# Kernel tuning notes

Measured on AMD Instinct MI355X. Metric: run time of the kernel, lower is better.

The kernel has to match this reference:

```python
import jax, jax.numpy as jnp
import numpy as np

N_NODES = 50000
IN_C = 128
OUT_C = 128
EDGE_F = 65
N_EDGES = 800000
EDGE_ATTR_COLS = 70


def setup_inputs() -> dict:
    key = jax.random.key(0)
    ks = jax.random.split(key, 10)
    fcat = 3 * IN_C + EDGE_F
    sc = lambda d: 1.0 / np.sqrt(d)
    return {
        "x": jax.random.normal(ks[0], (N_NODES, IN_C), dtype=jnp.float32),
        "edge_index": jax.random.randint(ks[1], (2, N_EDGES), 0, N_NODES, dtype=jnp.int32),
        "edge_attr": jax.random.normal(ks[2], (N_EDGES, EDGE_ATTR_COLS), dtype=jnp.float32),
        # f_linear: Linear(fcat -> IN_C, bias=True) followed by ELU
        "Wf": jax.random.normal(ks[3], (fcat, IN_C), dtype=jnp.float32) * sc(fcat),
        "bf": jnp.zeros((IN_C,), dtype=jnp.float32),
        # q/k linears: Linear(IN_C -> IN_C, bias=False)
        "Wq": jax.random.normal(ks[4], (IN_C, IN_C), dtype=jnp.float32) * sc(IN_C),
        "Wk": jax.random.normal(ks[5], (IN_C, IN_C), dtype=jnp.float32) * sc(IN_C),
        # alinear: Linear(IN_C -> 1, bias=False) + Tanh
        "Wa": jax.random.normal(ks[6], (IN_C, 1), dtype=jnp.float32) * sc(IN_C),
        # updatalinear: Linear(IN_C -> OUT_C, bias=True)
        "Wu": jax.random.normal(ks[7], (IN_C, OUT_C), dtype=jnp.float32) * sc(IN_C),
        "bu": jnp.zeros((OUT_C,), dtype=jnp.float32),
    }


def reference(x, edge_index, edge_attr, Wf, bf, Wq, Wk, Wa, Wu, bu):
    src = edge_index[0]
    tgt = edge_index[1]
    # message: gather endpoints, concat with delta and edge features, fuse MLP
    ni = x[src]                      # [E, C]
    nj = x[tgt]                      # [E, C]
    mask = (edge_attr[:, 0:1] < 8).astype(x.dtype)  # [E, 1]
    fcat = jnp.concatenate([ni, nj, ni - nj, edge_attr[:, :EDGE_F]], axis=1)
    f = jax.nn.elu(fcat @ Wf + bf) * mask           # [E, C]
    scale = IN_C ** (-0.5)
    q = ni @ Wq                                      # [E, C]
    k = f @ Wk                                       # [E, C]
    a = jnp.tanh((q * k * scale) @ Wa)               # [E, 1]
    # NOTE: faithful to source: denominator = exp(sum(a)), not sum(exp(a))
    numerator = jnp.exp(a)
    a_sum = jax.ops.segment_sum(a, src, num_segments=N_NODES)   # [N, 1]
    denominator = jnp.exp(a_sum)[src]                            # [E, 1]
    s = numerator / denominator
    z = s * f                                        # [E, C]
    # aggregate: scatter-sum over source nodes
    aggr = jax.ops.segment_sum(z, src, num_segments=N_NODES)     # [N, C]
    # update
    return (x + aggr) @ Wu + bu
```

## Files before the change

### kernel.cpp

```cpp
#include <hip/hip_runtime.h>

#define E_EDGES 800000
#define NN 50000
#define C 128
#define EAC 70
#define EF 65
#define SCALE 0.08838834764831845f

typedef __attribute__((ext_vector_type(8))) short short8;
typedef __attribute__((ext_vector_type(4))) float floatx4;

__device__ __forceinline__ unsigned short f2bf(float f) {
  unsigned u = __builtin_bit_cast(unsigned, f);
  unsigned r = (u + 0x7FFFu + ((u >> 16) & 1u)) >> 16;
  return (unsigned short)r;
}
__device__ __forceinline__ float bf2f(unsigned short h) {
  unsigned u = ((unsigned)h) << 16;
  return __builtin_bit_cast(float, u);
}

__global__ void setup_kernel(const float* __restrict__ Wf, const float* __restrict__ Wq,
                             const float* __restrict__ Wk, const float* __restrict__ Wa,
                             const int* __restrict__ src, unsigned short* __restrict__ wfrag,
                             float* __restrict__ Wm, int* __restrict__ deg) {
  int b = blockIdx.x;
  if (b < 64) {
    int idx = b * 256 + threadIdx.x;
    int r = idx >> 7, d = idx & 127;
    const float* wq = Wq + (size_t)r * C;
    const float* wk = Wk + (size_t)d * C;
    float s = 0.f;
    for (int c = 0; c < C; ++c) s += wq[c] * Wa[c] * wk[c];
    Wm[idx] = s * SCALE;
  } else if (b < 240) {
    int idx = (b - 64) * 256 + threadIdx.x;
    int arr = idx >> 14;
    int rem = idx & 16383;
    int j = rem & 7;
    int l = (rem >> 3) & 63;
    int st = rem >> 9;
    int s = st >> 3, t = st & 7;
    int k = s * 32 + (l >> 4) * 8 + j;
    int n = t * 16 + (l & 15);
    float v;
    if (arr == 0)      v = Wf[k * C + n] + Wf[(256 + k) * C + n];
    else if (arr == 1) v = Wf[(128 + k) * C + n] - Wf[(256 + k) * C + n];
    else               v = (k < EF) ? Wf[(384 + k) * C + n] : 0.f;
    wfrag[idx] = f2bf(v);
  } else {
    int e = (b - 240) * 256 + threadIdx.x;
    atomicAdd(deg + src[e], 1);
  }
}

__global__ __launch_bounds__(256) void m_kernel(const float* __restrict__ x,
                                                const float* __restrict__ Wm,
                                                unsigned short* __restrict__ M,
                                                unsigned short* __restrict__ XB) {
  __shared__ float rows[32][129];
  int b0 = blockIdx.x * 32;
  for (int idx = threadIdx.x; idx < 32 * 128; idx += 256) {
    int r = idx >> 7, i = idx & 127;
    int n = b0 + r;
    float v = 0.f;
    if (n < NN) {
      v = x[(size_t)n * C + i];
      XB[(size_t)n * C + i] = f2bf(v);
    }
    rows[r][i] = v;
  }
  __syncthreads();
  int tr = threadIdx.x >> 4;
  int tc = threadIdx.x & 15;
  floatx4 a00 = (floatx4){0,0,0,0}, a01 = a00, a10 = a00, a11 = a00;
  for (int i = 0; i < C; ++i) {
    float r0 = rows[tr * 2][i], r1 = rows[tr * 2 + 1][i];
    const floatx4* wr = (const floatx4*)(Wm + (size_t)i * C + tc * 8);
    floatx4 w0 = wr[0], w1 = wr[1];
    a00 += w0 * r0; a01 += w1 * r0;
    a10 += w0 * r1; a11 += w1 * r1;
  }
  int n0 = b0 + tr * 2;
  for (int rr = 0; rr < 2; ++rr) {
    int n = n0 + rr;
    if (n < NN) {
      floatx4 v0 = rr ? a10 : a00, v1 = rr ? a11 : a01;
      short8 o;
      for (int j = 0; j < 4; ++j) { o[j] = (short)f2bf(v0[j]); o[4 + j] = (short)f2bf(v1[j]); }
      *(short8*)(M + (size_t)n * C + tc * 8) = o;
    }
  }
}

__global__ __launch_bounds__(1024) void scan_kernel(const int* __restrict__ deg,
                                                    int* __restrict__ offs) {
  __shared__ int buf[1024];
  const int CH = 49;
  int t = threadIdx.x, base = t * CH;
  int s = 0;
  for (int k = 0; k < CH; ++k)
    if (base + k < NN) s += deg[base + k];
  buf[t] = s;
  __syncthreads();
  for (int d = 1; d < 1024; d <<= 1) {
    int add = (t >= d) ? buf[t - d] : 0;
    __syncthreads();
    buf[t] += add;
    __syncthreads();
  }
  int excl = buf[t] - s;
  for (int k = 0; k < CH; ++k)
    if (base + k < NN) { offs[base + k] = excl; excl += deg[base + k]; }
}

__global__ void pos_kernel(const int* __restrict__ src, const int* __restrict__ tgt,
                           const int* __restrict__ offs, int* __restrict__ cursor,
                           int* __restrict__ perm, int* __restrict__ srcs,
                           int* __restrict__ tgts) {
  int e = blockIdx.x * 256 + threadIdx.x;
  int r = src[e];
  int p = offs[r] + atomicAdd(cursor + r, 1);
  perm[p] = e;
  srcs[p] = r;
  tgts[p] = tgt[e];
}

__global__ __launch_bounds__(256, 5) void edge_kernel(
    const unsigned short* __restrict__ XB, const float* __restrict__ ea,
    const float* __restrict__ bfv, const unsigned short* __restrict__ wfrag,
    const int* __restrict__ perm, const int* __restrict__ srcs,
    const int* __restrict__ tgts, const unsigned short* __restrict__ M,
    unsigned short* __restrict__ Z, float* __restrict__ A) {
  __shared__ unsigned short f_lds[4][16][136];
  __shared__ float mask_lds[4][16];
  const int l = threadIdx.x & 63;
  const int w = threadIdx.x >> 6;
  const int lo = l & 15, quad = l >> 4;
  const int e0 = (blockIdx.x * 4 + w) * 16;

  const short8* WF1 = (const short8*)wfrag;
  const short8* WF2 = (const short8*)(wfrag + 16384);
  const short8* WF4 = (const short8*)(wfrag + 32768);

  int p = e0 + lo;
  int sp = srcs[p], tp = tgts[p], ep = perm[p];

  short8 niF[4], njF[4], eaF[3];
  {
    const short8* xr = (const short8*)(XB + (size_t)sp * C);
    const short8* yr = (const short8*)(XB + (size_t)tp * C);
    for (int s = 0; s < 4; ++s) { niF[s] = xr[s * 4 + quad]; njF[s] = yr[s * 4 + quad]; }
  }
  {
    const float* er = ea + (size_t)ep * EAC;
    const float2* ca = (const float2*)(er + quad * 8);
    const float2* cb = (const float2*)(er + 32 + quad * 8);
    float2 a0 = ca[0], a1 = ca[1], a2 = ca[2], a3 = ca[3];
    float2 b0 = cb[0], b1 = cb[1], b2 = cb[2], b3 = cb[3];
    short8 t0, t1, t2;
    t0[0] = (short)f2bf(a0.x); t0[1] = (short)f2bf(a0.y);
    t0[2] = (short)f2bf(a1.x); t0[3] = (short)f2bf(a1.y);
    t0[4] = (short)f2bf(a2.x); t0[5] = (short)f2bf(a2.y);
    t0[6] = (short)f2bf(a3.x); t0[7] = (short)f2bf(a3.y);
    t1[0] = (short)f2bf(b0.x); t1[1] = (short)f2bf(b0.y);
    t1[2] = (short)f2bf(b1.x); t1[3] = (short)f2bf(b1.y);
    t1[4] = (short)f2bf(b2.x); t1[5] = (short)f2bf(b2.y);
    t1[6] = (short)f2bf(b3.x); t1[7] = (short)f2bf(b3.y);
    for (int j = 0; j < 8; ++j) t2[j] = 0;
    if (quad == 0) {
      t2[0] = (short)f2bf(er[64]);
      mask_lds[w][lo] = (a0.x < 8.f) ? 1.f : 0.f;
    }
    eaF[0] = t0; eaF[1] = t1; eaF[2] = t2;
  }

  float maskv[4];
  int srcRow[4];
  for (int i = 0; i < 4; ++i) {
    maskv[i] = mask_lds[w][quad * 4 + i];
    srcRow[i] = srcs[e0 + quad * 4 + i];
  }

  for (int t = 0; t < 8; ++t) {
    floatx4 acc = (floatx4){0.f, 0.f, 0.f, 0.f};
    for (int s = 0; s < 4; ++s)
      acc = __builtin_amdgcn_mfma_f32_16x16x32_bf16(niF[s], WF1[(s * 8 + t) * 64 + l], acc, 0, 0, 0);
    for (int s = 0; s < 4; ++s)
      acc = __builtin_amdgcn_mfma_f32_16x16x32_bf16(njF[s], WF2[(s * 8 + t) * 64 + l], acc, 0, 0, 0);
    for (int s = 0; s < 3; ++s)
      acc = __builtin_amdgcn_mfma_f32_16x16x32_bf16(eaF[s], WF4[(s * 8 + t) * 64 + l], acc, 0, 0, 0);
    float bias = bfv[lo + 16 * t];
    for (int i = 0; i < 4; ++i) {
      float v = acc[i] + bias;
      v = v > 0.f ? v : expm1f(v);
      v *= maskv[i];
      f_lds[w][quad * 4 + i][lo + 16 * t] = f2bf(v);
    }
  }

  for (int i = 0; i < 4; ++i) {
    int pc = e0 + quad * 4 + i;
    const short8 fv = *(const short8*)&f_lds[w][quad * 4 + i][lo * 8];
    const short8 mv = *(const short8*)(M + (size_t)srcRow[i] * C + lo * 8);
    float d = 0.f;
    for (int j = 0; j < 8; ++j)
      d += bf2f((unsigned short)fv[j]) * bf2f((unsigned short)mv[j]);
    d += __shfl_xor(d, 1);
    d += __shfl_xor(d, 2);
    d += __shfl_xor(d, 4);
    d += __shfl_xor(d, 8);
    float a = tanhf(d);
    float cf = expf(a);
    short8 zv;
    for (int j = 0; j < 8; ++j) zv[j] = (short)f2bf(cf * bf2f((unsigned short)fv[j]));
    *(short8*)(Z + (size_t)pc * C + lo * 8) = zv;
    if (lo == 0) A[pc] = a;
  }
}

__global__ __launch_bounds__(256) void gather_node_kernel(
    const float* __restrict__ x, const unsigned short* __restrict__ Z,
    const float* __restrict__ A, const int* __restrict__ offs,
    const int* __restrict__ deg, const float* __restrict__ Wu,
    const float* __restrict__ bu, float* __restrict__ out) {
  __shared__ float rows[32][129];
  int b0 = blockIdx.x * 32;
  int w = threadIdx.x >> 6, l = threadIdx.x & 63;
  for (int r = w; r < 32; r += 4) {
    int n = b0 + r;
    if (n < NN) {
      int beg = offs[n], dn = deg[n];
      float ax = 0.f, ay = 0.f, asum = 0.f;
      const unsigned short* zp = Z + (size_t)beg * C + l * 2;
      const float* ap = A + beg;
      int j = 0;
      for (; j + 1 < dn; j += 2) {
        ushort2 z0 = *(const ushort2*)zp;
        ushort2 z1 = *(const ushort2*)(zp + C);
        zp += 2 * C;
        asum += ap[j] + ap[j + 1];
        ax += bf2f(z0.x) + bf2f(z1.x);
        ay += bf2f(z0.y) + bf2f(z1.y);
      }
      if (j < dn) {
        ushort2 z0 = *(const ushort2*)zp;
        asum += ap[j];
        ax += bf2f(z0.x); ay += bf2f(z0.y);
      }
      float cf = expf(-asum);
      rows[r][l * 2]     = x[(size_t)n * C + l * 2]     + cf * ax;
      rows[r][l * 2 + 1] = x[(size_t)n * C + l * 2 + 1] + cf * ay;
    } else {
      rows[r][l * 2] = 0.f;
      rows[r][l * 2 + 1] = 0.f;
    }
  }
  __syncthreads();
  int tr = threadIdx.x >> 4;
  int tc = threadIdx.x & 15;
  floatx4 a00 = (floatx4){0,0,0,0}, a01 = a00, a10 = a00, a11 = a00;
  for (int i = 0; i < C; ++i) {
    float r0 = rows[tr * 2][i], r1 = rows[tr * 2 + 1][i];
    const floatx4* wr = (const floatx4*)(Wu + (size_t)i * C + tc * 8);
    floatx4 w0 = wr[0], w1 = wr[1];
    a00 += w0 * r0; a01 += w1 * r0;
    a10 += w0 * r1; a11 += w1 * r1;
  }
  const floatx4* bv = (const floatx4*)(bu + tc * 8);
  floatx4 bb0 = bv[0], bb1 = bv[1];
  int n0 = b0 + tr * 2;
  if (n0 < NN) {
    floatx4* o = (floatx4*)(out + (size_t)n0 * C + tc * 8);
    o[0] = a00 + bb0; o[1] = a01 + bb1;
  }
  if (n0 + 1 < NN) {
    floatx4* o = (floatx4*)(out + (size_t)(n0 + 1) * C + tc * 8);
    o[0] = a10 + bb0; o[1] = a11 + bb1;
  }
}

__global__ __launch_bounds__(256, 4) void fb_edge_kernel(
    const float* __restrict__ x, const int* __restrict__ src,
    const int* __restrict__ tgt, const float* __restrict__ ea,
    const float* __restrict__ bfv, const unsigned short* __restrict__ wfrag,
    const unsigned short* __restrict__ M, float* __restrict__ a_sum,
    float* __restrict__ P) {
  __shared__ unsigned short f_lds[4][16][136];
  __shared__ float mask_lds[4][16];
  const int l = threadIdx.x & 63;
  const int w = threadIdx.x >> 6;
  const int lo = l & 15, quad = l >> 4;
  const int e0 = (blockIdx.x * 4 + w) * 16;
  const short8* WF1 = (const short8*)wfrag;
  const short8* WF2 = (const short8*)(wfrag + 16384);
  const short8* WF4 = (const short8*)(wfrag + 32768);

  int p = e0 + lo;
  int sp = src[p], tp = tgt[p];
  short8 niF[4], njF[4], eaF[3];
  {
    const float* xr = x + (size_t)sp * C;
    const float* yr = x + (size_t)tp * C;
    for (int s = 0; s < 4; ++s) {
      int kb = s * 32 + quad * 8;
      const floatx4* xv = (const floatx4*)(xr + kb);
      const floatx4* yv = (const floatx4*)(yr + kb);
      floatx4 x0 = xv[0], x1 = xv[1], y0 = yv[0], y1 = yv[1];
      short8 a, b;
      for (int j = 0; j < 4; ++j) { a[j] = (short)f2bf(x0[j]); a[4 + j] = (short)f2bf(x1[j]); }
      for (int j = 0; j < 4; ++j) { b[j] = (short)f2bf(y0[j]); b[4 + j] = (short)f2bf(y1[j]); }
      niF[s] = a; njF[s] = b;
    }
    const float* er = ea + (size_t)p * EAC;
    const float2* ca = (const float2*)(er + quad * 8);
    const float2* cb = (const float2*)(er + 32 + quad * 8);
    float2 a0 = ca[0], a1 = ca[1], a2 = ca[2], a3 = ca[3];
    float2 b0 = cb[0], b1 = cb[1], b2 = cb[2], b3 = cb[3];
    short8 t0, t1, t2;
    t0[0] = (short)f2bf(a0.x); t0[1] = (short)f2bf(a0.y);
    t0[2] = (short)f2bf(a1.x); t0[3] = (short)f2bf(a1.y);
    t0[4] = (short)f2bf(a2.x); t0[5] = (short)f2bf(a2.y);
    t0[6] = (short)f2bf(a3.x); t0[7] = (short)f2bf(a3.y);
    t1[0] = (short)f2bf(b0.x); t1[1] = (short)f2bf(b0.y);
    t1[2] = (short)f2bf(b1.x); t1[3] = (short)f2bf(b1.y);
    t1[4] = (short)f2bf(b2.x); t1[5] = (short)f2bf(b2.y);
    t1[6] = (short)f2bf(b3.x); t1[7] = (short)f2bf(b3.y);
    for (int j = 0; j < 8; ++j) t2[j] = 0;
    if (quad == 0) {
      t2[0] = (short)f2bf(er[64]);
      mask_lds[w][lo] = (a0.x < 8.f) ? 1.f : 0.f;
    }
    eaF[0] = t0; eaF[1] = t1; eaF[2] = t2;
  }
  float maskv[4];
  int srcRow[4];
  for (int i = 0; i < 4; ++i) {
    maskv[i] = mask_lds[w][quad * 4 + i];
    srcRow[i] = src[e0 + quad * 4 + i];
  }
  for (int t = 0; t < 8; ++t) {
    floatx4 acc = (floatx4){0.f, 0.f, 0.f, 0.f};
    for (int s = 0; s < 4; ++s)
      acc = __builtin_amdgcn_mfma_f32_16x16x32_bf16(niF[s], WF1[(s * 8 + t) * 64 + l], acc, 0, 0, 0);
    for (int s = 0; s < 4; ++s)
      acc = __builtin_amdgcn_mfma_f32_16x16x32_bf16(njF[s], WF2[(s * 8 + t) * 64 + l], acc, 0, 0, 0);
    for (int s = 0; s < 3; ++s)
      acc = __builtin_amdgcn_mfma_f32_16x16x32_bf16(eaF[s], WF4[(s * 8 + t) * 64 + l], acc, 0, 0, 0);
    float bias = bfv[lo + 16 * t];
    for (int i = 0; i < 4; ++i) {
      float v = acc[i] + bias;
      v = v > 0.f ? v : expm1f(v);
      v *= maskv[i];
      f_lds[w][quad * 4 + i][lo + 16 * t] = f2bf(v);
    }
  }
  for (int i = 0; i < 4; ++i) {
    const short8 fv = *(const short8*)&f_lds[w][quad * 4 + i][lo * 8];
    const short8 mv = *(const short8*)(M + (size_t)srcRow[i] * C + lo * 8);
    float d = 0.f;
    for (int j = 0; j < 8; ++j)
      d += bf2f((unsigned short)fv[j]) * bf2f((unsigned short)mv[j]);
    d += __shfl_xor(d, 1);
    d += __shfl_xor(d, 2);
    d += __shfl_xor(d, 4);
    d += __shfl_xor(d, 8);
    float a = tanhf(d);
    float cf = expf(a);
    if (lo == 0) atomicAdd(a_sum + srcRow[i], a);
    float* Prow = P + (size_t)srcRow[i] * C;
    for (int j = 0; j < 8; ++j)
      atomicAdd(Prow + lo * 8 + j, cf * bf2f((unsigned short)fv[j]));
  }
}

__global__ __launch_bounds__(256) void fb_node_kernel(
    const float* __restrict__ x, const float* __restrict__ P,
    const float* __restrict__ a_sum, const float* __restrict__ Wu,
    const float* __restrict__ bu, float* __restrict__ out) {
  __shared__ float rows[32][129];
  int b0 = blockIdx.x * 32;
  for (int idx = threadIdx.x; idx < 32 * 128; idx += 256) {
    int r = idx >> 7, i = idx & 127;
    int n = b0 + r;
    float v = 0.f;
    if (n < NN) v = x[(size_t)n * C + i] + expf(-a_sum[n]) * P[(size_t)n * C + i];
    rows[r][i] = v;
  }
  __syncthreads();
  int tr = threadIdx.x >> 4;
  int tc = threadIdx.x & 15;
  floatx4 a00 = (floatx4){0,0,0,0}, a01 = a00, a10 = a00, a11 = a00;
  for (int i = 0; i < C; ++i) {
    float r0 = rows[tr * 2][i], r1 = rows[tr * 2 + 1][i];
    const floatx4* wr = (const floatx4*)(Wu + (size_t)i * C + tc * 8);
    floatx4 w0 = wr[0], w1 = wr[1];
    a00 += w0 * r0; a01 += w1 * r0;
    a10 += w0 * r1; a11 += w1 * r1;
  }
  const floatx4* bv = (const floatx4*)(bu + tc * 8);
  floatx4 bb0 = bv[0], bb1 = bv[1];
  int n0 = b0 + tr * 2;
  if (n0 < NN) {
    floatx4* o = (floatx4*)(out + (size_t)n0 * C + tc * 8);
    o[0] = a00 + bb0; o[1] = a01 + bb1;
  }
  if (n0 + 1 < NN) {
    floatx4* o = (floatx4*)(out + (size_t)(n0 + 1) * C + tc * 8);
    o[0] = a10 + bb0; o[1] = a11 + bb1;
  }
}

extern "C" void kernel_launch(void* const* d_in, const int* in_sizes, int n_in,
                              void* d_out, int out_size, void* d_ws, size_t ws_size,
                              hipStream_t stream) {
  const float* x  = (const float*)d_in[0];
  const int*   ei = (const int*)d_in[1];
  const float* ea = (const float*)d_in[2];
  const float* Wf = (const float*)d_in[3];
  const float* bf = (const float*)d_in[4];
  const float* Wq = (const float*)d_in[5];
  const float* Wk = (const float*)d_in[6];
  const float* Wa = (const float*)d_in[7];
  const float* Wu = (const float*)d_in[8];
  const float* bu = (const float*)d_in[9];
  float* out = (float*)d_out;
  const int* src = ei;
  const int* tgt = ei + E_EDGES;

  size_t off = 0;
  auto take = [&](size_t n) { size_t r = off; off += (n + 255) & ~(size_t)255; return r; };
  size_t oZ    = take((size_t)E_EDGES * C * 2);
  size_t oDeg  = take((size_t)NN * 4);
  size_t oCur  = take((size_t)NN * 4);
  size_t oOffs = take((size_t)NN * 4);
  size_t oPerm = take((size_t)E_EDGES * 4);
  size_t oSrcs = take((size_t)E_EDGES * 4);
  size_t oTgts = take((size_t)E_EDGES * 4);
  size_t oWfr  = take((size_t)45056 * 2);
  size_t oWm   = take((size_t)C * C * 4);
  size_t oM    = take((size_t)NN * C * 2);
  size_t oXB   = take((size_t)NN * C * 2);
  size_t oA    = take((size_t)E_EDGES * 4);
  size_t need = off;

  if (ws_size >= need) {
    unsigned short* Z = (unsigned short*)((char*)d_ws + oZ);
    int* deg = (int*)((char*)d_ws + oDeg);
    int* cursor = (int*)((char*)d_ws + oCur);
    int* offs = (int*)((char*)d_ws + oOffs);
    int* perm = (int*)((char*)d_ws + oPerm);
    int* srcs = (int*)((char*)d_ws + oSrcs);
    int* tgts = (int*)((char*)d_ws + oTgts);
    unsigned short* wfrag = (unsigned short*)((char*)d_ws + oWfr);
    float* Wm = (float*)((char*)d_ws + oWm);
    unsigned short* M = (unsigned short*)((char*)d_ws + oM);
    unsigned short* XB = (unsigned short*)((char*)d_ws + oXB);
    float* A = (float*)((char*)d_ws + oA);

    hipMemsetAsync(deg, 0, oOffs - oDeg, stream);
    setup_kernel<<<3365, 256, 0, stream>>>(Wf, Wq, Wk, Wa, src, wfrag, Wm, deg);
    m_kernel<<<(NN + 31) / 32, 256, 0, stream>>>(x, Wm, M, XB);
    scan_kernel<<<1, 1024, 0, stream>>>(deg, offs);
    pos_kernel<<<E_EDGES / 256, 256, 0, stream>>>(src, tgt, offs, cursor, perm, srcs, tgts);
    edge_kernel<<<E_EDGES / 64, 256, 0, stream>>>(XB, ea, bf, wfrag, perm, srcs, tgts,
                                                  M, Z, A);
    gather_node_kernel<<<(NN + 31) / 32, 256, 0, stream>>>(x, Z, A, offs, deg, Wu, bu, out);
  } else {
    size_t f = 0;
    auto tk = [&](size_t n) { size_t r = f; f += (n + 255) & ~(size_t)255; return r; };
    size_t fP = tk((size_t)NN * C * 4);
    size_t fAs = tk((size_t)NN * 4);
    size_t fDeg = tk((size_t)NN * 4);
    size_t fWfr = tk((size_t)45056 * 2);
    size_t fWm = tk((size_t)C * C * 4);
    size_t fM = tk((size_t)NN * C * 2);
    float* P = (float*)((char*)d_ws + fP);
    float* a_sum = (float*)((char*)d_ws + fAs);
    int* deg = (int*)((char*)d_ws + fDeg);
    unsigned short* wfrag = (unsigned short*)((char*)d_ws + fWfr);
    float* Wm = (float*)((char*)d_ws + fWm);
    unsigned short* M = (unsigned short*)((char*)d_ws + fM);
    hipMemsetAsync(P, 0, (size_t)NN * C * 4 + 256 + NN * 4, stream);
    setup_kernel<<<3365, 256, 0, stream>>>(Wf, Wq, Wk, Wa, src, wfrag, Wm, deg);
    m_kernel<<<(NN + 31) / 32, 256, 0, stream>>>(x, Wm, M, (unsigned short*)P);
    hipMemsetAsync(P, 0, (size_t)NN * C * 4, stream);
    fb_edge_kernel<<<E_EDGES / 64, 256, 0, stream>>>(x, src, tgt, ea, bf, wfrag, M,
                                                     a_sum, P);
    fb_node_kernel<<<(NN + 31) / 32, 256, 0, stream>>>(x, P, a_sum, Wu, bu, out);
  }
}
```

Before: 900.9 us.

## Fuse segment aggregation into edge kernel via sorted-run atomics

The edge kernel no longer writes per-edge Z and A arrays to global memory for a separate gather pass. Edges are already sorted by source, so each wave reduces consecutive same-source rows held in LDS and issues one atomicAdd per run into a per-node P and a_sum. The gather pass becomes a simple node kernel that reads P. This removes about 200MB of bf16 Z writes and reads, in exchange for float atomics, a memset of P, and non-deterministic summation order.

```diff
diff --git a/kernel.cpp b/kernel.cpp
--- a/kernel.cpp
+++ b/kernel.cpp
@@ -131,9 +131,11 @@
     const float* __restrict__ bfv, const unsigned short* __restrict__ wfrag,
     const int* __restrict__ perm, const int* __restrict__ srcs,
     const int* __restrict__ tgts, const unsigned short* __restrict__ M,
-    unsigned short* __restrict__ Z, float* __restrict__ A) {
+    float* __restrict__ P, float* __restrict__ a_sum) {
   __shared__ unsigned short f_lds[4][16][136];
   __shared__ float mask_lds[4][16];
+  __shared__ float a_lds[4][16];
+  __shared__ int src_lds[4][16];
   const int l = threadIdx.x & 63;
   const int w = threadIdx.x >> 6;
   const int lo = l & 15, quad = l >> 4;
@@ -145,6 +147,7 @@
 
   int p = e0 + lo;
   int sp = srcs[p], tp = tgts[p], ep = perm[p];
+  if (l < 16) src_lds[w][l] = sp;
 
   short8 niF[4], njF[4], eaF[3];
   {
@@ -179,7 +182,7 @@
   int srcRow[4];
   for (int i = 0; i < 4; ++i) {
     maskv[i] = mask_lds[w][quad * 4 + i];
-    srcRow[i] = srcs[e0 + quad * 4 + i];
+    srcRow[i] = src_lds[w][quad * 4 + i];
   }
 
   for (int t = 0; t < 8; ++t) {
@@ -200,7 +203,6 @@
   }
 
   for (int i = 0; i < 4; ++i) {
-    int pc = e0 + quad * 4 + i;
     const short8 fv = *(const short8*)&f_lds[w][quad * 4 + i][lo * 8];
     const short8 mv = *(const short8*)(M + (size_t)srcRow[i] * C + lo * 8);
     float d = 0.f;
@@ -214,47 +216,49 @@
     float cf = expf(a);
     short8 zv;
     for (int j = 0; j < 8; ++j) zv[j] = (short)f2bf(cf * bf2f((unsigned short)fv[j]));
-    *(short8*)(Z + (size_t)pc * C + lo * 8) = zv;
-    if (lo == 0) A[pc] = a;
-  }
-}
-
-__global__ __launch_bounds__(256) void gather_node_kernel(
-    const float* __restrict__ x, const unsigned short* __restrict__ Z,
-    const float* __restrict__ A, const int* __restrict__ offs,
-    const int* __restrict__ deg, const float* __restrict__ Wu,
+    *(short8*)&f_lds[w][quad * 4 + i][lo * 8] = zv;
+    if (lo == 0) a_lds[w][quad * 4 + i] = a;
+  }
+
+  {
+    const int col = l << 1;
+    float acc0 = 0.f, acc1 = 0.f, accA = 0.f;
+    int cur = __builtin_amdgcn_readfirstlane(src_lds[w][0]);
+#pragma unroll
+    for (int r = 0; r < 16; ++r) {
+      int s_r = __builtin_amdgcn_readfirstlane(src_lds[w][r]);
+      if (s_r != cur) {
+        float* pr = P + (size_t)cur * C + col;
+        atomicAdd(pr, acc0);
+        atomicAdd(pr + 1, acc1);
+        if (l == 0) atomicAdd(a_sum + cur, accA);
+        acc0 = acc1 = accA = 0.f;
+        cur = s_r;
+      }
+      unsigned v = *(const unsigned*)&f_lds[w][r][col];
+      acc0 += bf2f((unsigned short)(v & 0xFFFFu));
+      acc1 += bf2f((unsigned short)(v >> 16));
+      accA += a_lds[w][r];
+    }
+    float* pr = P + (size_t)cur * C + col;
+    atomicAdd(pr, acc0);
+    atomicAdd(pr + 1, acc1);
+    if (l == 0) atomicAdd(a_sum + cur, accA);
+  }
+}
+
+__global__ __launch_bounds__(256) void node_kernel(
+    const float* __restrict__ x, const float* __restrict__ P,
+    const float* __restrict__ a_sum, const float* __restrict__ Wu,
     const float* __restrict__ bu, float* __restrict__ out) {
   __shared__ float rows[32][129];
   int b0 = blockIdx.x * 32;
-  int w = threadIdx.x >> 6, l = threadIdx.x & 63;
-  for (int r = w; r < 32; r += 4) {
+  for (int idx = threadIdx.x; idx < 32 * 128; idx += 256) {
+    int r = idx >> 7, i = idx & 127;
     int n = b0 + r;
-    if (n < NN) {
-      int beg = offs[n], dn = deg[n];
-      float ax = 0.f, ay = 0.f, asum = 0.f;
-      const unsigned short* zp = Z + (size_t)beg * C + l * 2;
-      const float* ap = A + beg;
-      int j = 0;
-      for (; j + 1 < dn; j += 2) {
-        ushort2 z0 = *(const ushort2*)zp;
-        ushort2 z1 = *(const ushort2*)(zp + C);
-        zp += 2 * C;
-        asum += ap[j] + ap[j + 1];
-        ax += bf2f(z0.x) + bf2f(z1.x);
-        ay += bf2f(z0.y) + bf2f(z1.y);
-      }
-      if (j < dn) {
-        ushort2 z0 = *(const ushort2*)zp;
-        asum += ap[j];
-        ax += bf2f(z0.x); ay += bf2f(z0.y);
-      }
-      float cf = expf(-asum);
-      rows[r][l * 2]     = x[(size_t)n * C + l * 2]     + cf * ax;
-      rows[r][l * 2 + 1] = x[(size_t)n * C + l * 2 + 1] + cf * ay;
-    } else {
-      rows[r][l * 2] = 0.f;
-      rows[r][l * 2 + 1] = 0.f;
-    }
+    float v = 0.f;
+    if (n < NN) v = x[(size_t)n * C + i] + expf(-a_sum[n]) * P[(size_t)n * C + i];
+    rows[r][i] = v;
   }
   __syncthreads();
   int tr = threadIdx.x >> 4;
@@ -374,43 +378,6 @@
   }
 }
 
-__global__ __launch_bounds__(256) void fb_node_kernel(
-    const float* __restrict__ x, const float* __restrict__ P,
-    const float* __restrict__ a_sum, const float* __restrict__ Wu,
-    const float* __restrict__ bu, float* __restrict__ out) {
-  __shared__ float rows[32][129];
-  int b0 = blockIdx.x * 32;
-  for (int idx = threadIdx.x; idx < 32 * 128; idx += 256) {
-    int r = idx >> 7, i = idx & 127;
-    int n = b0 + r;
-    float v = 0.f;
-    if (n < NN) v = x[(size_t)n * C + i] + expf(-a_sum[n]) * P[(size_t)n * C + i];
-    rows[r][i] = v;
-  }
-  __syncthreads();
-  int tr = threadIdx.x >> 4;
-  int tc = threadIdx.x & 15;
-  floatx4 a00 = (floatx4){0,0,0,0}, a01 = a00, a10 = a00, a11 = a00;
-  for (int i = 0; i < C; ++i) {
-    float r0 = rows[tr * 2][i], r1 = rows[tr * 2 + 1][i];
-    const floatx4* wr = (const floatx4*)(Wu + (size_t)i * C + tc * 8);
-    floatx4 w0 = wr[0], w1 = wr[1];
-    a00 += w0 * r0; a01 += w1 * r0;
-    a10 += w0 * r1; a11 += w1 * r1;
-  }
-  const floatx4* bv = (const floatx4*)(bu + tc * 8);
-  floatx4 bb0 = bv[0], bb1 = bv[1];
-  int n0 = b0 + tr * 2;
-  if (n0 < NN) {
-    floatx4* o = (floatx4*)(out + (size_t)n0 * C + tc * 8);
-    o[0] = a00 + bb0; o[1] = a01 + bb1;
-  }
-  if (n0 + 1 < NN) {
-    floatx4* o = (floatx4*)(out + (size_t)(n0 + 1) * C + tc * 8);
-    o[0] = a10 + bb0; o[1] = a11 + bb1;
-  }
-}
-
 extern "C" void kernel_launch(void* const* d_in, const int* in_sizes, int n_in,
                               void* d_out, int out_size, void* d_ws, size_t ws_size,
                               hipStream_t stream) {
@@ -430,7 +397,8 @@
 
   size_t off = 0;
   auto take = [&](size_t n) { size_t r = off; off += (n + 255) & ~(size_t)255; return r; };
-  size_t oZ    = take((size_t)E_EDGES * C * 2);
+  size_t oP    = take((size_t)NN * C * 4);
+  size_t oAs   = take((size_t)NN * 4);
   size_t oDeg  = take((size_t)NN * 4);
   size_t oCur  = take((size_t)NN * 4);
   size_t oOffs = take((size_t)NN * 4);
@@ -441,11 +409,11 @@
   size_t oWm   = take((size_t)C * C * 4);
   size_t oM    = take((size_t)NN * C * 2);
   size_t oXB   = take((size_t)NN * C * 2);
-  size_t oA    = take((size_t)E_EDGES * 4);
   size_t need = off;
 
   if (ws_size >= need) {
-    unsigned short* Z = (unsigned short*)((char*)d_ws + oZ);
+    float* P = (float*)((char*)d_ws + oP);
+    float* a_sum = (float*)((char*)d_ws + oAs);
     int* deg = (int*)((char*)d_ws + oDeg);
     int* cursor = (int*)((char*)d_ws + oCur);
     int* offs = (int*)((char*)d_ws + oOffs);
@@ -456,16 +424,15 @@
     float* Wm = (float*)((char*)d_ws + oWm);
     unsigned short* M = (unsigned short*)((char*)d_ws + oM);
     unsigned short* XB = (unsigned short*)((char*)d_ws + oXB);
-    float* A = (float*)((char*)d_ws + oA);
-
-    hipMemsetAsync(deg, 0, oOffs - oDeg, stream);
+
+    hipMemsetAsync(P, 0, oOffs - oP, stream);
     setup_kernel<<<3365, 256, 0, stream>>>(Wf, Wq, Wk, Wa, src, wfrag, Wm, deg);
     m_kernel<<<(NN + 31) / 32, 256, 0, stream>>>(x, Wm, M, XB);
     scan_kernel<<<1, 1024, 0, stream>>>(deg, offs);
     pos_kernel<<<E_EDGES / 256, 256, 0, stream>>>(src, tgt, offs, cursor, perm, srcs, tgts);
     edge_kernel<<<E_EDGES / 64, 256, 0, stream>>>(XB, ea, bf, wfrag, perm, srcs, tgts,
-                                                  M, Z, A);
-    gather_node_kernel<<<(NN + 31) / 32, 256, 0, stream>>>(x, Z, A, offs, deg, Wu, bu, out);
+                                                  M, P, a_sum);
+    node_kernel<<<(NN + 31) / 32, 256, 0, stream>>>(x, P, a_sum, Wu, bu, out);
   } else {
     size_t f = 0;
     auto tk = [&](size_t n) { size_t r = f; f += (n + 255) & ~(size_t)255; return r; };
@@ -487,6 +454,6 @@
     hipMemsetAsync(P, 0, (size_t)NN * C * 4, stream);
     fb_edge_kernel<<<E_EDGES / 64, 256, 0, stream>>>(x, src, tgt, ea, bf, wfrag, M,
                                                      a_sum, P);
-    fb_node_kernel<<<(NN + 31) / 32, 256, 0, stream>>>(x, P, a_sum, Wu, bu, out);
-  }
-}
+    node_kernel<<<(NN + 31) / 32, 256, 0, stream>>>(x, P, a_sum, Wu, bu, out);
+  }
+}
```

New measurement: 884.5 us. About the same (-1.8%).
